# Kernel tuning notes

Hardware: AMD Instinct MI355X
Metric: run time of the kernel (lower is better)

The kernel has to match this reference:

```python
import jax, jax.numpy as jnp
import numpy as np

B, T = 1, 1024
V, E, H, HKV, DH = 32000, 1024, 16, 4, 64
L, R = 2, 2            # n_layer, n_recurrent
ROPE = 32              # head_dim * rotary_pct (0.5)
EPS = 1e-5


def _layer_norm(x, g, b):
    mu = jnp.mean(x, axis=-1, keepdims=True)
    var = jnp.mean((x - mu) ** 2, axis=-1, keepdims=True)
    return (x - mu) * jax.lax.rsqrt(var + EPS) * g + b


def _rotate_half(x):
    x1, x2 = jnp.split(x, 2, axis=-1)
    return jnp.concatenate([-x2, x1], axis=-1)


def _rope_cache(t):
    theta = 1.0 / (10000.0 ** (jnp.arange(0, ROPE, 2, dtype=jnp.float32) / ROPE))
    freqs = jnp.arange(t, dtype=jnp.float32)[:, None] * theta[None, :]  # [t, ROPE/2]
    cos = jnp.concatenate([jnp.cos(freqs), jnp.cos(freqs)], axis=-1)    # [t, ROPE]
    sin = jnp.concatenate([jnp.sin(freqs), jnp.sin(freqs)], axis=-1)
    return cos, sin


def _attn(x, Wq, Wk, Wv, Wo, gate, cos, sin):
    b, t, c = x.shape
    q = (x @ Wq).reshape(b, t, H, DH).transpose(0, 2, 1, 3)     # [b,H,t,D]
    k = (x @ Wk).reshape(b, t, HKV, DH).transpose(0, 2, 1, 3)   # [b,Hkv,t,D]
    v = (x @ Wv).reshape(b, t, HKV, DH).transpose(0, 2, 1, 3)
    c4, s4 = cos[None, None, :t, :], sin[None, None, :t, :]
    q_r, q_p = q[..., :ROPE], q[..., ROPE:]
    k_r, k_p = k[..., :ROPE], k[..., ROPE:]
    q = jnp.concatenate([q_r * c4 + _rotate_half(q_r) * s4, q_p], axis=-1)
    k = jnp.concatenate([k_r * c4 + _rotate_half(k_r) * s4, k_p], axis=-1)
    # GQA: repeat kv heads
    k = jnp.repeat(k, H // HKV, axis=1)
    v = jnp.repeat(v, H // HKV, axis=1)
    att = jnp.einsum('bhtd,bhsd->bhts', q, k) * (DH ** -0.5)
    causal = jnp.tril(jnp.ones((t, t), dtype=bool))
    att = jnp.where(causal[None, None], att, -jnp.inf)
    att = jax.nn.softmax(att, axis=-1)
    # learned per-head sigmoid-threshold sparsifying gate
    thr = jax.nn.sigmoid(gate)[None, :, None, None]
    att = att * (att >= thr).astype(att.dtype)
    y = jnp.einsum('bhts,bhsd->bhtd', att, v).transpose(0, 2, 1, 3).reshape(b, t, c)
    return y @ Wo


def reference(embed, ln1_g, ln1_b, Wq, Wk, Wv, Wo, gate, ln2_g, ln2_b, W1, W2, lnf_g, lnf_b, idx, targets):
    x = embed[idx]                      # [B,T,E]
    cos, sin = _rope_cache(T)
    for _ in range(R):
        for l in range(L):
            x = x + _attn(_layer_norm(x, ln1_g[l], ln1_b[l]), Wq[l], Wk[l], Wv[l], Wo[l], gate[l], cos, sin)
            h = _layer_norm(x, ln2_g[l], ln2_b[l])
            x = x + jax.nn.gelu(h @ W1[l], approximate=False) @ W2[l]
    x = _layer_norm(x, lnf_g, lnf_b)
    logits = x @ embed.T                # tied lm_head
    logp = jax.nn.log_softmax(logits, axis=-1)
    loss = -jnp.mean(jnp.take_along_axis(logp, targets[..., None], axis=-1))
    return logits, loss


def setup_inputs():
    key = jax.random.key(0)
    ks = jax.random.split(key, 9)
    s = 0.02
    return {
        'embed': jax.random.normal(ks[0], (V, E), jnp.float32) * s,
        'ln1_g': jnp.ones((L, E), jnp.float32), 'ln1_b': jnp.zeros((L, E), jnp.float32),
        'Wq': jax.random.normal(ks[1], (L, E, E), jnp.float32) * s,
        'Wk': jax.random.normal(ks[2], (L, E, HKV * DH), jnp.float32) * s,
        'Wv': jax.random.normal(ks[3], (L, E, HKV * DH), jnp.float32) * s,
        'Wo': jax.random.normal(ks[4], (L, E, E), jnp.float32) * s,
        'gate': jnp.zeros((L, H), jnp.float32),
        'ln2_g': jnp.ones((L, E), jnp.float32), 'ln2_b': jnp.zeros((L, E), jnp.float32),
        'W1': jax.random.normal(ks[5], (L, E, 4 * E), jnp.float32) * s,
        'W2': jax.random.normal(ks[6], (L, 4 * E, E), jnp.float32) * s,
        'lnf_g': jnp.ones((E,), jnp.float32), 'lnf_b': jnp.zeros((E,), jnp.float32),
        'idx': jax.random.randint(ks[7], (B, T), 0, V, dtype=jnp.int32),
        'targets': jax.random.randint(ks[8], (B, T), 0, V, dtype=jnp.int32),
    }
```

## Files before the change

### kernel.cpp

```cpp
#include <hip/hip_runtime.h>
#include <math.h>

#define TT 1024
#define VV 32000
#define EE 1024
#define NH 16
#define NKVH 4
#define DHEAD 64
#define QKVN 1536
#define FF 4096
#define LEPS 1e-5f

typedef __attribute__((ext_vector_type(8))) short short8;
typedef __attribute__((ext_vector_type(4))) float floatx4;

__device__ __forceinline__ ushort f2bf(float f) {
    unsigned x = __float_as_uint(f);
    unsigned r = (x + 0x7fffu + ((x >> 16) & 1u)) >> 16;
    return (ushort)r;
}
__device__ __forceinline__ float bf2f(ushort u) {
    return __uint_as_float(((unsigned)u) << 16);
}

__device__ __forceinline__ float block_reduce_sum(float v, float* red) {
    int tid = threadIdx.x;
    red[tid] = v; __syncthreads();
    for (int off = 128; off > 0; off >>= 1) {
        if (tid < off) red[tid] += red[tid + off];
        __syncthreads();
    }
    float r = red[0];
    __syncthreads();
    return r;
}
__device__ __forceinline__ float block_reduce_max(float v, float* red) {
    int tid = threadIdx.x;
    red[tid] = v; __syncthreads();
    for (int off = 128; off > 0; off >>= 1) {
        if (tid < off) red[tid] = fmaxf(red[tid], red[tid + off]);
        __syncthreads();
    }
    float r = red[0];
    __syncthreads();
    return r;
}

__global__ __launch_bounds__(256) void convert_bf16_kernel(const float* __restrict__ src,
                                                           ushort* __restrict__ dst, long n4) {
    long i = (long)blockIdx.x * 256 + threadIdx.x;
    if (i >= n4) return;
    float4 f = ((const float4*)src)[i];
    ushort u[4] = { f2bf(f.x), f2bf(f.y), f2bf(f.z), f2bf(f.w) };
    ((uint2*)dst)[i] = *(uint2*)u;
}

__global__ __launch_bounds__(256) void transpose_bf16_kernel(const float* __restrict__ W,
                                                             ushort* __restrict__ dst,
                                                             int N, int K) {
    __shared__ float tile[32][33];
    int n0 = blockIdx.x * 32, k0 = blockIdx.y * 32;
    int tx = threadIdx.x & 31, ty = threadIdx.x >> 5;
    for (int i = ty; i < 32; i += 8) tile[i][tx] = W[(long)(k0 + i) * N + n0 + tx];
    __syncthreads();
    for (int i = ty; i < 32; i += 8)
        dst[(long)(n0 + i) * K + k0 + tx] = f2bf(tile[tx][i]);
}

__global__ __launch_bounds__(256) void gather_kernel(const float* __restrict__ embed,
                                                     const int* __restrict__ idx,
                                                     float* __restrict__ x) {
    int t = blockIdx.x;
    long r = idx[t];
    const float4* src = (const float4*)(embed + r * EE);
    float4* dst = (float4*)(x + (long)t * EE);
    for (int i = threadIdx.x; i < EE / 4; i += 256) dst[i] = src[i];
}

__global__ __launch_bounds__(256) void ln_kernel(const float* __restrict__ x,
                                                 const float* __restrict__ g,
                                                 const float* __restrict__ b,
                                                 ushort* __restrict__ out) {
    __shared__ float red[256];
    int t = blockIdx.x;
    const float* xr = x + (long)t * EE;
    float s = 0.f;
    for (int i = threadIdx.x; i < EE; i += 256) s += xr[i];
    float mu = block_reduce_sum(s, red) * (1.f / EE);
    float vs = 0.f;
    for (int i = threadIdx.x; i < EE; i += 256) { float d = xr[i] - mu; vs += d * d; }
    float var = block_reduce_sum(vs, red) * (1.f / EE);
    float rstd = rsqrtf(var + LEPS);
    ushort* orow = out + (long)t * EE;
    for (int i = threadIdx.x; i < EE; i += 256)
        orow[i] = f2bf((xr[i] - mu) * rstd * g[i] + b[i]);
}

__global__ __launch_bounds__(256) void reduce_ln_kernel(const float* __restrict__ part,
                                                        float* __restrict__ x,
                                                        const float* __restrict__ g,
                                                        const float* __restrict__ b,
                                                        ushort* __restrict__ out, int SK) {
    __shared__ float red[256];
    int t = blockIdx.x;
    int tid = threadIdx.x;
    float4 v = ((const float4*)(x + (long)t * EE))[tid];
    for (int k = 0; k < SK; ++k) {
        float4 pp = ((const float4*)(part + (long)k * TT * EE + (long)t * EE))[tid];
        v.x += pp.x; v.y += pp.y; v.z += pp.z; v.w += pp.w;
    }
    ((float4*)(x + (long)t * EE))[tid] = v;
    float s = v.x + v.y + v.z + v.w;
    float mu = block_reduce_sum(s, red) * (1.f / EE);
    float d0 = v.x - mu, d1 = v.y - mu, d2 = v.z - mu, d3 = v.w - mu;
    float vs = d0 * d0 + d1 * d1 + d2 * d2 + d3 * d3;
    float var = block_reduce_sum(vs, red) * (1.f / EE);
    float rstd = rsqrtf(var + LEPS);
    float4 gg = ((const float4*)g)[tid];
    float4 bb = ((const float4*)b)[tid];
    ushort4 o;
    o.x = f2bf(d0 * rstd * gg.x + bb.x);
    o.y = f2bf(d1 * rstd * gg.y + bb.y);
    o.z = f2bf(d2 * rstd * gg.z + bb.z);
    o.w = f2bf(d3 * rstd * gg.w + bb.w);
    ((ushort4*)(out + (long)t * EE))[tid] = o;
}

#define M_QKV    0
#define M_FF1    1
#define M_PART   2
#define M_LMHEAD 3

template<int MODE>
__global__ __launch_bounds__(256) void gemm_bf16(const ushort* __restrict__ A,
                                                 const ushort* __restrict__ B,
                                                 void* __restrict__ Cv,
                                                 float* __restrict__ lstats,
                                                 int M, int N, int K) {
    __shared__ char lds[16384];
    const int tid = threadIdx.x;
    const int lane = tid & 63;
    const int w = tid >> 6;

    const int nwg = gridDim.x;
    const int lin = blockIdx.x;
    const int q8 = nwg >> 3, r8 = nwg & 7;
    const int xcd = lin & 7, loc = lin >> 3;
    const int wg = (xcd < r8 ? xcd * (q8 + 1) : r8 * (q8 + 1) + (xcd - r8) * q8) + loc;
    const int MB = M >> 7;
    const int row0 = (wg % MB) * 128;
    const int col0 = (wg / MB) * 128;

    const int nsl = gridDim.y;
    const int kslice = K / nsl;
    const long koff = (long)blockIdx.y * kslice;

    const char* ga[2]; const char* gb[2];
    char* la[2]; char* lb[2];
    #pragma unroll
    for (int r = 0; r < 2; ++r) {
        int c = r * 256 + tid;
        ga[r] = (const char*)A + ((long)(row0 + (c >> 2)) * K + koff) * 2 + (c & 3) * 16;
        gb[r] = (const char*)B + ((long)(col0 + (c >> 2)) * K + koff) * 2 + (c & 3) * 16;
        int wc = r * 256 + w * 64;
        la[r] = lds + wc * 16;
        lb[r] = lds + 8192 + wc * 16;
    }

    floatx4 acc[4][4];
    #pragma unroll
    for (int i = 0; i < 4; ++i)
        #pragma unroll
        for (int j = 0; j < 4; ++j) acc[i][j] = {0.f, 0.f, 0.f, 0.f};

    const int mbase = (w >> 1) * 64;
    const int nbase = (w & 1) * 64;
    const int lr = lane & 15;
    const int ko = (lane >> 4) * 16;

    for (int k0 = 0; k0 < kslice; k0 += 32) {
        #pragma unroll
        for (int r = 0; r < 2; ++r) {
            __builtin_amdgcn_global_load_lds(
                (const __attribute__((address_space(1))) void*)ga[r],
                (__attribute__((address_space(3))) void*)la[r], 16, 0, 0);
            __builtin_amdgcn_global_load_lds(
                (const __attribute__((address_space(1))) void*)gb[r],
                (__attribute__((address_space(3))) void*)lb[r], 16, 0, 0);
            ga[r] += 64; gb[r] += 64;
        }
        __syncthreads();
        short8 af[4], bfr[4];
        #pragma unroll
        for (int i = 0; i < 4; ++i)
            af[i] = *(const short8*)(lds + (mbase + i * 16 + lr) * 64 + ko);
        #pragma unroll
        for (int j = 0; j < 4; ++j)
            bfr[j] = *(const short8*)(lds + 8192 + (nbase + j * 16 + lr) * 64 + ko);
        #pragma unroll
        for (int i = 0; i < 4; ++i)
            #pragma unroll
            for (int j = 0; j < 4; ++j)
                acc[i][j] = __builtin_amdgcn_mfma_f32_16x16x32_bf16(af[i], bfr[j], acc[i][j], 0, 0, 0);
        __syncthreads();
    }

    const int orow = (lane >> 4) * 4;
    const int ocol = lane & 15;

    if (MODE == M_QKV && (col0 + nbase) < (EE + NKVH * DHEAD)) {
        float th = expf(-(float)ocol * 0.5756462732485114f);
        #pragma unroll
        for (int i = 0; i < 4; ++i)
            #pragma unroll
            for (int r = 0; r < 4; ++r) {
                float ang = (float)(row0 + mbase + i * 16 + orow + r) * th;
                float c = cosf(ang), s = sinf(ang);
                float a = acc[i][0][r], bb = acc[i][1][r];
                acc[i][0][r] = a * c - bb * s;
                acc[i][1][r] = bb * c + a * s;
            }
    }

    #pragma unroll
    for (int i = 0; i < 4; ++i) {
        #pragma unroll
        for (int j = 0; j < 4; ++j) {
            #pragma unroll
            for (int r = 0; r < 4; ++r) {
                long off = (long)(row0 + mbase + i * 16 + orow + r) * N
                         + (col0 + nbase + j * 16 + ocol);
                float v = acc[i][j][r];
                if (MODE == M_FF1) v = 0.5f * v * (1.f + erff(v * 0.70710678118654752f));
                if (MODE == M_QKV || MODE == M_FF1) {
                    ((ushort*)Cv)[off] = f2bf(v);
                } else {
                    ((float*)Cv + (long)blockIdx.y * (long)M * N)[off] = v;
                }
            }
        }
    }

    if (MODE == M_LMHEAD) {
        float rm[4][4], rs[4][4];
        #pragma unroll
        for (int i = 0; i < 4; ++i)
            #pragma unroll
            for (int r = 0; r < 4; ++r) {
                float m0 = fmaxf(fmaxf(acc[i][0][r], acc[i][1][r]),
                                 fmaxf(acc[i][2][r], acc[i][3][r]));
                float s0 = expf(acc[i][0][r] - m0) + expf(acc[i][1][r] - m0)
                         + expf(acc[i][2][r] - m0) + expf(acc[i][3][r] - m0);
                #pragma unroll
                for (int off = 1; off < 16; off <<= 1) {
                    float om = __shfl_xor(m0, off);
                    float os = __shfl_xor(s0, off);
                    float nm = fmaxf(m0, om);
                    s0 = s0 * expf(m0 - nm) + os * expf(om - nm);
                    m0 = nm;
                }
                rm[i][r] = m0; rs[i][r] = s0;
            }
        float2* msb = (float2*)lds;
        if (ocol == 0) {
            #pragma unroll
            for (int i = 0; i < 4; ++i)
                #pragma unroll
                for (int r = 0; r < 4; ++r)
                    msb[w * 64 + i * 16 + orow + r] = make_float2(rm[i][r], rs[i][r]);
        }
        __syncthreads();
        if (tid < 128) {
            int half = tid >> 6, rloc = tid & 63;
            float2 a = msb[(half * 2) * 64 + rloc];
            float2 bq = msb[(half * 2 + 1) * 64 + rloc];
            float nm = fmaxf(a.x, bq.x);
            float ns = a.y * expf(a.x - nm) + bq.y * expf(bq.x - nm);
            ((float2*)lstats)[(long)(row0 + half * 64 + rloc) * (N >> 7) + (col0 >> 7)]
                = make_float2(nm, ns);
        }
    }
}

__global__ __launch_bounds__(256) void scores_gemm(const ushort* __restrict__ qkv,
                                                   float* __restrict__ scores) {
    __shared__ char lds[16384];
    const int tid = threadIdx.x;
    const int lane = tid & 63;
    const int w = tid >> 6;
    const int col0 = blockIdx.x * 128, row0 = blockIdx.y * 128, h = blockIdx.z;
    if (col0 > row0) return;

    const ushort* A = qkv + h * DHEAD;
    const ushort* B = qkv + EE + (h >> 2) * DHEAD;

    const char* ga[2]; const char* gb[2];
    char* la[2]; char* lb[2];
    #pragma unroll
    for (int r = 0; r < 2; ++r) {
        int c = r * 256 + tid;
        ga[r] = (const char*)A + (long)(row0 + (c >> 2)) * QKVN * 2 + (c & 3) * 16;
        gb[r] = (const char*)B + (long)(col0 + (c >> 2)) * QKVN * 2 + (c & 3) * 16;
        int wc = r * 256 + w * 64;
        la[r] = lds + wc * 16;
        lb[r] = lds + 8192 + wc * 16;
    }

    floatx4 acc[4][4];
    #pragma unroll
    for (int i = 0; i < 4; ++i)
        #pragma unroll
        for (int j = 0; j < 4; ++j) acc[i][j] = {0.f, 0.f, 0.f, 0.f};

    const int mbase = (w >> 1) * 64;
    const int nbase = (w & 1) * 64;
    const int lr = lane & 15;
    const int ko = (lane >> 4) * 16;

    for (int k0 = 0; k0 < DHEAD; k0 += 32) {
        #pragma unroll
        for (int r = 0; r < 2; ++r) {
            __builtin_amdgcn_global_load_lds(
                (const __attribute__((address_space(1))) void*)ga[r],
                (__attribute__((address_space(3))) void*)la[r], 16, 0, 0);
            __builtin_amdgcn_global_load_lds(
                (const __attribute__((address_space(1))) void*)gb[r],
                (__attribute__((address_space(3))) void*)lb[r], 16, 0, 0);
            ga[r] += 64; gb[r] += 64;
        }
        __syncthreads();
        short8 af[4], bfr[4];
        #pragma unroll
        for (int i = 0; i < 4; ++i)
            af[i] = *(const short8*)(lds + (mbase + i * 16 + lr) * 64 + ko);
        #pragma unroll
        for (int j = 0; j < 4; ++j)
            bfr[j] = *(const short8*)(lds + 8192 + (nbase + j * 16 + lr) * 64 + ko);
        #pragma unroll
        for (int i = 0; i < 4; ++i)
            #pragma unroll
            for (int j = 0; j < 4; ++j)
                acc[i][j] = __builtin_amdgcn_mfma_f32_16x16x32_bf16(af[i], bfr[j], acc[i][j], 0, 0, 0);
        __syncthreads();
    }

    float* C = scores + (long)h * TT * TT;
    const int orow = (lane >> 4) * 4;
    const int ocol = lane & 15;
    #pragma unroll
    for (int i = 0; i < 4; ++i)
        #pragma unroll
        for (int j = 0; j < 4; ++j)
            #pragma unroll
            for (int r = 0; r < 4; ++r)
                C[(long)(row0 + mbase + i * 16 + orow + r) * TT
                  + (col0 + nbase + j * 16 + ocol)] = acc[i][j][r];
}

__global__ __launch_bounds__(256) void softmax_gate_kernel(float* __restrict__ scores,
                                                           const float* __restrict__ gate) {
    int h = blockIdx.x;
    int t = blockIdx.y * 4 + (threadIdx.x >> 6);
    int lane = threadIdx.x & 63;
    float* row = scores + (long)h * TT * TT + (long)t * TT;

    float4 v[4];
    float lmax = -INFINITY;
    #pragma unroll
    for (int q = 0; q < 4; ++q) {
        int u = lane + q * 64;
        v[q] = ((const float4*)row)[u];
        int s0 = u * 4;
        v[q].x = (s0 + 0 <= t) ? v[q].x * 0.125f : -INFINITY;
        v[q].y = (s0 + 1 <= t) ? v[q].y * 0.125f : -INFINITY;
        v[q].z = (s0 + 2 <= t) ? v[q].z * 0.125f : -INFINITY;
        v[q].w = (s0 + 3 <= t) ? v[q].w * 0.125f : -INFINITY;
        lmax = fmaxf(lmax, fmaxf(fmaxf(v[q].x, v[q].y), fmaxf(v[q].z, v[q].w)));
    }
    #pragma unroll
    for (int off = 1; off < 64; off <<= 1)
        lmax = fmaxf(lmax, __shfl_xor(lmax, off));

    float e[16];
    float lsum = 0.f;
    #pragma unroll
    for (int q = 0; q < 4; ++q) {
        e[q * 4 + 0] = expf(v[q].x - lmax);
        e[q * 4 + 1] = expf(v[q].y - lmax);
        e[q * 4 + 2] = expf(v[q].z - lmax);
        e[q * 4 + 3] = expf(v[q].w - lmax);
        lsum += e[q * 4 + 0] + e[q * 4 + 1] + e[q * 4 + 2] + e[q * 4 + 3];
    }
    #pragma unroll
    for (int off = 1; off < 64; off <<= 1)
        lsum += __shfl_xor(lsum, off);

    float inv = 1.f / lsum;
    float thr = 1.f / (1.f + expf(-gate[h]));
    ushort* prow = (ushort*)row;
    #pragma unroll
    for (int q = 0; q < 4; ++q) {
        ushort4 o;
        float p;
        p = e[q * 4 + 0] * inv; o.x = f2bf(p >= thr ? p : 0.f);
        p = e[q * 4 + 1] * inv; o.y = f2bf(p >= thr ? p : 0.f);
        p = e[q * 4 + 2] * inv; o.z = f2bf(p >= thr ? p : 0.f);
        p = e[q * 4 + 3] * inv; o.w = f2bf(p >= thr ? p : 0.f);
        ((ushort4*)prow)[lane + q * 64] = o;
    }
}

__global__ __launch_bounds__(256) void vtrans_kernel(const ushort* __restrict__ qkv,
                                                     ushort* __restrict__ VT) {
    __shared__ ushort tile[32][33];
    int s0 = blockIdx.x * 32, d0 = blockIdx.y * 32;
    int tx = threadIdx.x & 31, ty = threadIdx.x >> 5;
    for (int i = ty; i < 32; i += 8)
        tile[i][tx] = qkv[(long)(s0 + i) * QKVN + (EE + NKVH * DHEAD) + d0 + tx];
    __syncthreads();
    for (int i = ty; i < 32; i += 8)
        VT[(long)(d0 + i) * TT + s0 + tx] = tile[tx][i];
}

__global__ __launch_bounds__(256) void pv_gemm(const float* __restrict__ scores,
                                               const ushort* __restrict__ VT,
                                               ushort* __restrict__ y) {
    __shared__ char lds[12288];
    const int tid = threadIdx.x;
    const int lane = tid & 63;
    const int w = tid >> 6;
    const int row0 = blockIdx.x * 128, h = blockIdx.y;

    const char* Pb = (const char*)(scores + (long)h * TT * TT);
    const char* Bv = (const char*)(VT + (long)(h >> 2) * DHEAD * TT);

    const char* ga[2]; char* la[2];
    #pragma unroll
    for (int r = 0; r < 2; ++r) {
        int c = r * 256 + tid;
        ga[r] = Pb + (long)(row0 + (c >> 2)) * 4096 + (c & 3) * 16;
        la[r] = lds + (r * 256 + w * 64) * 16;
    }
    const char* gb = Bv + (long)(tid >> 2) * 2048 + (tid & 3) * 16;
    char* lb = lds + 8192 + (w * 64) * 16;

    floatx4 acc[2][4];
    #pragma unroll
    for (int i = 0; i < 2; ++i)
        #pragma unroll
        for (int j = 0; j < 4; ++j) acc[i][j] = {0.f, 0.f, 0.f, 0.f};

    const int mbase = w * 32;
    const int lr = lane & 15;
    const int ko = (lane >> 4) * 16;

    const int kmax = row0 + 128;
    for (int k0 = 0; k0 < kmax; k0 += 32) {
        #pragma unroll
        for (int r = 0; r < 2; ++r) {
            __builtin_amdgcn_global_load_lds(
                (const __attribute__((address_space(1))) void*)ga[r],
                (__attribute__((address_space(3))) void*)la[r], 16, 0, 0);
            ga[r] += 64;
        }
        __builtin_amdgcn_global_load_lds(
            (const __attribute__((address_space(1))) void*)gb,
            (__attribute__((address_space(3))) void*)lb, 16, 0, 0);
        gb += 64;
        __syncthreads();
        short8 af[2], bfr[4];
        #pragma unroll
        for (int i = 0; i < 2; ++i)
            af[i] = *(const short8*)(lds + (mbase + i * 16 + lr) * 64 + ko);
        #pragma unroll
        for (int j = 0; j < 4; ++j)
            bfr[j] = *(const short8*)(lds + 8192 + (j * 16 + lr) * 64 + ko);
        #pragma unroll
        for (int i = 0; i < 2; ++i)
            #pragma unroll
            for (int j = 0; j < 4; ++j)
                acc[i][j] = __builtin_amdgcn_mfma_f32_16x16x32_bf16(af[i], bfr[j], acc[i][j], 0, 0, 0);
        __syncthreads();
    }

    const int orow = (lane >> 4) * 4;
    const int ocol = lane & 15;
    #pragma unroll
    for (int i = 0; i < 2; ++i)
        #pragma unroll
        for (int j = 0; j < 4; ++j)
            #pragma unroll
            for (int r = 0; r < 4; ++r)
                y[(long)(row0 + mbase + i * 16 + orow + r) * EE
                  + h * DHEAD + j * 16 + ocol] = f2bf(acc[i][j][r]);
}

__global__ __launch_bounds__(64) void row_loss_kernel(const float* __restrict__ logits,
                                                      const float* __restrict__ lstats,
                                                      const int* __restrict__ targets,
                                                      float* __restrict__ row_loss) {
    int t = blockIdx.x;
    int lane = threadIdx.x;
    const float2* st = (const float2*)lstats + (long)t * (VV / 128);
    float m = -INFINITY, s = 0.f;
    for (int i = lane; i < VV / 128; i += 64) {
        float2 v = st[i];
        float nm = fmaxf(m, v.x);
        s = s * expf(m - nm) + v.y * expf(v.x - nm);
        m = nm;
    }
    #pragma unroll
    for (int off = 1; off < 64; off <<= 1) {
        float om = __shfl_xor(m, off);
        float os = __shfl_xor(s, off);
        float nm = fmaxf(m, om);
        s = s * expf(m - nm) + os * expf(om - nm);
        m = nm;
    }
    if (lane == 0)
        row_loss[t] = logf(s) + m - logits[(long)t * VV + targets[t]];
}

__global__ __launch_bounds__(256) void final_loss_kernel(const float* __restrict__ row_loss,
                                                         float* __restrict__ out) {
    __shared__ float red[256];
    float s = 0.f;
    for (int i = threadIdx.x; i < TT; i += 256) s += row_loss[i];
    float tot = block_reduce_sum(s, red);
    if (threadIdx.x == 0) out[0] = tot * (1.f / TT);
}

extern "C" void kernel_launch(void* const* d_in, const int* in_sizes, int n_in,
                              void* d_out, int out_size, void* d_ws, size_t ws_size,
                              hipStream_t stream) {
    const float* embed = (const float*)d_in[0];
    const float* ln1_g = (const float*)d_in[1];
    const float* ln1_b = (const float*)d_in[2];
    const float* Wq    = (const float*)d_in[3];
    const float* Wk    = (const float*)d_in[4];
    const float* Wv    = (const float*)d_in[5];
    const float* Wo    = (const float*)d_in[6];
    const float* gate  = (const float*)d_in[7];
    const float* ln2_g = (const float*)d_in[8];
    const float* ln2_b = (const float*)d_in[9];
    const float* W1    = (const float*)d_in[10];
    const float* W2    = (const float*)d_in[11];
    const float* lnf_g = (const float*)d_in[12];
    const float* lnf_b = (const float*)d_in[13];
    const int*   idx   = (const int*)d_in[14];
    const int*   tgt   = (const int*)d_in[15];
    float* out = (float*)d_out;

    char* p = (char*)d_ws;
    float*  x      = (float*)p;  p += (long)TT * EE * 4;
    ushort* xn     = (ushort*)p; p += (long)TT * EE * 2;
    ushort* qkvb   = (ushort*)p; p += (long)TT * QKVN * 2;
    ushort* y      = (ushort*)p; p += (long)TT * EE * 2;
    ushort* h1     = (ushort*)p; p += (long)TT * FF * 2;
    float*  rls    = (float*)p;  p += (long)TT * 4;
    ushort* VT     = (ushort*)p; p += (long)NKVH * DHEAD * TT * 2;
    float*  scores = (float*)p;  p += (long)NH * TT * TT * 4;
    ushort* wqkvT  = (ushort*)p; p += (long)2 * QKVN * EE * 2;
    ushort* woT    = (ushort*)p; p += (long)2 * EE * EE * 2;
    ushort* w1T    = (ushort*)p; p += (long)2 * FF * EE * 2;
    ushort* w2T    = (ushort*)p; p += (long)2 * EE * FF * 2;
    ushort* embB   = (ushort*)p; p += (long)VV * EE * 2;

    float* gpart = scores;

    convert_bf16_kernel<<<((long)VV * EE / 4 + 255) / 256, 256, 0, stream>>>(embed, embB, (long)VV * EE / 4);
    for (int l = 0; l < 2; ++l) {
        transpose_bf16_kernel<<<dim3(EE / 32, EE / 32), 256, 0, stream>>>(
            Wq + (long)l * EE * EE, wqkvT + (long)l * QKVN * EE, EE, EE);
        transpose_bf16_kernel<<<dim3(NKVH * DHEAD / 32, EE / 32), 256, 0, stream>>>(
            Wk + (long)l * EE * NKVH * DHEAD, wqkvT + (long)l * QKVN * EE + (long)EE * EE, NKVH * DHEAD, EE);
        transpose_bf16_kernel<<<dim3(NKVH * DHEAD / 32, EE / 32), 256, 0, stream>>>(
            Wv + (long)l * EE * NKVH * DHEAD, wqkvT + (long)l * QKVN * EE + (long)(EE + NKVH * DHEAD) * EE, NKVH * DHEAD, EE);
        transpose_bf16_kernel<<<dim3(EE / 32, EE / 32), 256, 0, stream>>>(
            Wo + (long)l * EE * EE, woT + (long)l * EE * EE, EE, EE);
        transpose_bf16_kernel<<<dim3(FF / 32, EE / 32), 256, 0, stream>>>(
            W1 + (long)l * EE * FF, w1T + (long)l * FF * EE, FF, EE);
        transpose_bf16_kernel<<<dim3(EE / 32, FF / 32), 256, 0, stream>>>(
            W2 + (long)l * FF * EE, w2T + (long)l * EE * FF, EE, FF);
    }

    gather_kernel<<<TT, 256, 0, stream>>>(embed, idx, x);
    ln_kernel<<<TT, 256, 0, stream>>>(x, ln1_g, ln1_b, xn);

    for (int r = 0; r < 2; ++r) {
        for (int l = 0; l < 2; ++l) {
            gemm_bf16<M_QKV><<<dim3((TT / 128) * (QKVN / 128)), 256, 0, stream>>>(
                xn, wqkvT + (long)l * QKVN * EE, qkvb, nullptr, TT, QKVN, EE);
            vtrans_kernel<<<dim3(TT / 32, NKVH * DHEAD / 32), 256, 0, stream>>>(qkvb, VT);
            scores_gemm<<<dim3(TT / 128, TT / 128, NH), 256, 0, stream>>>(qkvb, scores);
            softmax_gate_kernel<<<dim3(NH, TT / 4), 256, 0, stream>>>(scores, gate + l * NH);
            pv_gemm<<<dim3(TT / 128, NH), 256, 0, stream>>>(scores, VT, y);

            gemm_bf16<M_PART><<<dim3((TT / 128) * (EE / 128), 2), 256, 0, stream>>>(
                y, woT + (long)l * EE * EE, gpart, nullptr, TT, EE, EE);
            reduce_ln_kernel<<<TT, 256, 0, stream>>>(
                gpart, x, ln2_g + l * EE, ln2_b + l * EE, xn, 2);

            gemm_bf16<M_FF1><<<dim3((TT / 128) * (FF / 128)), 256, 0, stream>>>(
                xn, w1T + (long)l * FF * EE, h1, nullptr, TT, FF, EE);

            gemm_bf16<M_PART><<<dim3((TT / 128) * (EE / 128), 4), 256, 0, stream>>>(
                h1, w2T + (long)l * EE * FF, gpart, nullptr, TT, EE, FF);
            const float* gn; const float* bn;
            if (r == 1 && l == 1) { gn = lnf_g; bn = lnf_b; }
            else { int lnx = (l == 0) ? 1 : 0; gn = ln1_g + lnx * EE; bn = ln1_b + lnx * EE; }
            reduce_ln_kernel<<<TT, 256, 0, stream>>>(gpart, x, gn, bn, xn, 4);
        }
    }

    gemm_bf16<M_LMHEAD><<<dim3((TT / 128) * (VV / 128)), 256, 0, stream>>>(
        xn, embB, out, gpart, TT, VV, EE);

    row_loss_kernel<<<TT, 64, 0, stream>>>(out, gpart, tgt, rls);
    final_loss_kernel<<<1, 256, 0, stream>>>(rls, out + (long)TT * VV);
}
```

Baseline: 1.186 ms.

## Add dedicated 256x256-tile LM-head GEMM with fused softmax stats

Replaces the generic 128x128 GEMM used for the LM head with a dedicated 512-thread kernel that computes 256x256 tiles. It double-buffers 64-wide K slices into 128KB of LDS via direct global-to-LDS loads with XOR swizzling, and raises wave priority around the MFMA blocks. The per-tile row max and sum-exp are reduced across four column-waves in LDS, giving 125 stats per row instead of 250. The larger tiles raise arithmetic intensity and cut redundant operand reads for the vocabulary GEMM, which is the largest single GEMM here. In exchange the kernel uses heavy LDS and registers, which limits occupancy.

```diff
diff --git a/kernel.cpp b/kernel.cpp
--- a/kernel.cpp
+++ b/kernel.cpp
@@ -129,13 +129,11 @@
 #define M_QKV    0
 #define M_FF1    1
 #define M_PART   2
-#define M_LMHEAD 3
 
 template<int MODE>
 __global__ __launch_bounds__(256) void gemm_bf16(const ushort* __restrict__ A,
                                                  const ushort* __restrict__ B,
                                                  void* __restrict__ Cv,
-                                                 float* __restrict__ lstats,
                                                  int M, int N, int K) {
     __shared__ char lds[16384];
     const int tid = threadIdx.x;
@@ -240,46 +238,156 @@
             }
         }
     }
-
-    if (MODE == M_LMHEAD) {
-        float rm[4][4], rs[4][4];
-        #pragma unroll
-        for (int i = 0; i < 4; ++i)
-            #pragma unroll
-            for (int r = 0; r < 4; ++r) {
-                float m0 = fmaxf(fmaxf(acc[i][0][r], acc[i][1][r]),
-                                 fmaxf(acc[i][2][r], acc[i][3][r]));
-                float s0 = expf(acc[i][0][r] - m0) + expf(acc[i][1][r] - m0)
-                         + expf(acc[i][2][r] - m0) + expf(acc[i][3][r] - m0);
-                #pragma unroll
-                for (int off = 1; off < 16; off <<= 1) {
-                    float om = __shfl_xor(m0, off);
-                    float os = __shfl_xor(s0, off);
-                    float nm = fmaxf(m0, om);
-                    s0 = s0 * expf(m0 - nm) + os * expf(om - nm);
-                    m0 = nm;
-                }
-                rm[i][r] = m0; rs[i][r] = s0;
+}
+
+__global__ __launch_bounds__(512, 2) void lmhead_gemm256(const ushort* __restrict__ A,
+                                                         const ushort* __restrict__ B,
+                                                         float* __restrict__ C,
+                                                         float* __restrict__ lstats) {
+    __shared__ char lds[131072];
+    const int tid = threadIdx.x;
+    const int lane = tid & 63;
+    const int w = tid >> 6;
+    const int wr = w >> 2;
+    const int wc = w & 3;
+
+    const int nwg = gridDim.x;
+    const int lin = blockIdx.x;
+    const int q8 = nwg >> 3, r8 = nwg & 7;
+    const int xcd = lin & 7, loc = lin >> 3;
+    const int wg = (xcd < r8 ? xcd * (q8 + 1) : r8 * (q8 + 1) + (xcd - r8) * q8) + loc;
+    const int row0 = (wg & 3) * 256;
+    const int col0 = (wg >> 2) * 256;
+
+    const int NT = EE / 64;
+
+    const int aB2 = (wr * 128 + (lane & 15)) * 128;
+    const int bB2 = (wc * 64 + (lane & 15)) * 128;
+    const int ks0 = ((0 * 4 + (lane >> 4)) ^ (lane & 7)) * 16;
+    const int ks1 = ((1 * 4 + (lane >> 4)) ^ (lane & 7)) * 16;
+
+    const int sRow = tid >> 3;
+    const int sSlotX = tid & 7;
+
+    floatx4 acc[8][4];
+    #pragma unroll
+    for (int i = 0; i < 8; ++i)
+        #pragma unroll
+        for (int j = 0; j < 4; ++j) acc[i][j] = {0.f, 0.f, 0.f, 0.f};
+
+    #define STAGE256(kt, bufsel)                                                     \
+    do {                                                                             \
+        _Pragma("unroll")                                                            \
+        for (int i = 0; i < 4; ++i) {                                                \
+            int rowD = i * 64 + sRow;                                                \
+            int slotSw = sSlotX ^ (rowD & 7);                                        \
+            const char* gsrc = (const char*)A + (long)(row0 + rowD) * 2048           \
+                             + (kt) * 128 + slotSw * 16;                             \
+            char* ldst = lds + (bufsel) * 32768 + i * 8192 + tid * 16;               \
+            __builtin_amdgcn_global_load_lds(                                        \
+                (const __attribute__((address_space(1))) void*)gsrc,                 \
+                (__attribute__((address_space(3))) void*)ldst, 16, 0, 0);            \
+        }                                                                            \
+        _Pragma("unroll")                                                            \
+        for (int i = 0; i < 4; ++i) {                                                \
+            int rowD = i * 64 + sRow;                                                \
+            int slotSw = sSlotX ^ (rowD & 7);                                        \
+            const char* gsrc = (const char*)B + (long)(col0 + rowD) * 2048           \
+                             + (kt) * 128 + slotSw * 16;                             \
+            char* ldst = lds + 65536 + (bufsel) * 32768 + i * 8192 + tid * 16;       \
+            __builtin_amdgcn_global_load_lds(                                        \
+                (const __attribute__((address_space(1))) void*)gsrc,                 \
+                (__attribute__((address_space(3))) void*)ldst, 16, 0, 0);            \
+        }                                                                            \
+    } while (0)
+
+    STAGE256(0, 0);
+    STAGE256(1, 1);
+    asm volatile("s_waitcnt vmcnt(8)" ::: "memory");
+    __builtin_amdgcn_s_barrier();
+    __builtin_amdgcn_sched_barrier(0);
+
+    for (int kt = 0; kt < NT; ++kt) {
+        const char* Ab = lds + (kt & 1) * 32768;
+        const char* Bb = lds + 65536 + (kt & 1) * 32768;
+
+        short8 bfr[4][2];
+        #pragma unroll
+        for (int fn = 0; fn < 4; ++fn) {
+            bfr[fn][0] = *(const short8*)(Bb + bB2 + fn * 2048 + ks0);
+            bfr[fn][1] = *(const short8*)(Bb + bB2 + fn * 2048 + ks1);
+        }
+        __builtin_amdgcn_s_setprio(1);
+        #pragma unroll
+        for (int fm = 0; fm < 8; ++fm) {
+            short8 a0 = *(const short8*)(Ab + aB2 + fm * 2048 + ks0);
+            short8 a1 = *(const short8*)(Ab + aB2 + fm * 2048 + ks1);
+            #pragma unroll
+            for (int fn = 0; fn < 4; ++fn) {
+                acc[fm][fn] = __builtin_amdgcn_mfma_f32_16x16x32_bf16(a0, bfr[fn][0], acc[fm][fn], 0, 0, 0);
+                acc[fm][fn] = __builtin_amdgcn_mfma_f32_16x16x32_bf16(a1, bfr[fn][1], acc[fm][fn], 0, 0, 0);
             }
-        float2* msb = (float2*)lds;
-        if (ocol == 0) {
-            #pragma unroll
-            for (int i = 0; i < 4; ++i)
-                #pragma unroll
-                for (int r = 0; r < 4; ++r)
-                    msb[w * 64 + i * 16 + orow + r] = make_float2(rm[i][r], rs[i][r]);
-        }
-        __syncthreads();
-        if (tid < 128) {
-            int half = tid >> 6, rloc = tid & 63;
-            float2 a = msb[(half * 2) * 64 + rloc];
-            float2 bq = msb[(half * 2 + 1) * 64 + rloc];
-            float nm = fmaxf(a.x, bq.x);
-            float ns = a.y * expf(a.x - nm) + bq.y * expf(bq.x - nm);
-            ((float2*)lstats)[(long)(row0 + half * 64 + rloc) * (N >> 7) + (col0 >> 7)]
-                = make_float2(nm, ns);
-        }
-    }
+        }
+        __builtin_amdgcn_s_setprio(0);
+
+        if (kt == NT - 1) break;
+
+        asm volatile("s_waitcnt lgkmcnt(0)" ::: "memory");
+        __builtin_amdgcn_s_barrier();
+        __builtin_amdgcn_sched_barrier(0);
+        if (kt + 2 < NT) {
+            STAGE256(kt + 2, kt & 1);
+            asm volatile("s_waitcnt vmcnt(8)" ::: "memory");
+        } else {
+            asm volatile("s_waitcnt vmcnt(0)" ::: "memory");
+        }
+        __builtin_amdgcn_s_barrier();
+        __builtin_amdgcn_sched_barrier(0);
+    }
+    #undef STAGE256
+
+    __syncthreads();
+    float2* msb = (float2*)lds;
+    #pragma unroll
+    for (int fm = 0; fm < 8; ++fm) {
+        #pragma unroll
+        for (int r = 0; r < 4; ++r) {
+            float m0 = fmaxf(fmaxf(acc[fm][0][r], acc[fm][1][r]),
+                             fmaxf(acc[fm][2][r], acc[fm][3][r]));
+            #pragma unroll
+            for (int off = 1; off < 16; off <<= 1)
+                m0 = fmaxf(m0, __shfl_xor(m0, off));
+            float s0 = expf(acc[fm][0][r] - m0) + expf(acc[fm][1][r] - m0)
+                     + expf(acc[fm][2][r] - m0) + expf(acc[fm][3][r] - m0);
+            #pragma unroll
+            for (int off = 1; off < 16; off <<= 1)
+                s0 += __shfl_xor(s0, off);
+            if ((lane & 15) == 0)
+                msb[wc * 256 + wr * 128 + fm * 16 + (lane >> 4) * 4 + r] = make_float2(m0, s0);
+        }
+    }
+    __syncthreads();
+    if (tid < 256) {
+        float2 v = msb[tid];
+        float m = v.x, s = v.y;
+        #pragma unroll
+        for (int q = 1; q < 4; ++q) {
+            float2 u = msb[q * 256 + tid];
+            float nm = fmaxf(m, u.x);
+            s = s * expf(m - nm) + u.y * expf(u.x - nm);
+            m = nm;
+        }
+        ((float2*)lstats)[(long)(row0 + tid) * 125 + (col0 >> 8)] = make_float2(m, s);
+    }
+
+    #pragma unroll
+    for (int fm = 0; fm < 8; ++fm)
+        #pragma unroll
+        for (int fn = 0; fn < 4; ++fn)
+            #pragma unroll
+            for (int r = 0; r < 4; ++r)
+                C[(long)(row0 + wr * 128 + fm * 16 + (lane >> 4) * 4 + r) * VV
+                  + col0 + wc * 64 + fn * 16 + (lane & 15)] = acc[fm][fn][r];
 }
 
 __global__ __launch_bounds__(256) void scores_gemm(const ushort* __restrict__ qkv,
@@ -501,9 +609,9 @@
                                                       float* __restrict__ row_loss) {
     int t = blockIdx.x;
     int lane = threadIdx.x;
-    const float2* st = (const float2*)lstats + (long)t * (VV / 128);
+    const float2* st = (const float2*)lstats + (long)t * 125;
     float m = -INFINITY, s = 0.f;
-    for (int i = lane; i < VV / 128; i += 64) {
+    for (int i = lane; i < 125; i += 64) {
         float2 v = st[i];
         float nm = fmaxf(m, v.x);
         s = s * expf(m - nm) + v.y * expf(v.x - nm);
@@ -590,22 +698,22 @@
     for (int r = 0; r < 2; ++r) {
         for (int l = 0; l < 2; ++l) {
             gemm_bf16<M_QKV><<<dim3((TT / 128) * (QKVN / 128)), 256, 0, stream>>>(
-                xn, wqkvT + (long)l * QKVN * EE, qkvb, nullptr, TT, QKVN, EE);
+                xn, wqkvT + (long)l * QKVN * EE, qkvb, TT, QKVN, EE);
             vtrans_kernel<<<dim3(TT / 32, NKVH * DHEAD / 32), 256, 0, stream>>>(qkvb, VT);
             scores_gemm<<<dim3(TT / 128, TT / 128, NH), 256, 0, stream>>>(qkvb, scores);
             softmax_gate_kernel<<<dim3(NH, TT / 4), 256, 0, stream>>>(scores, gate + l * NH);
             pv_gemm<<<dim3(TT / 128, NH), 256, 0, stream>>>(scores, VT, y);
 
             gemm_bf16<M_PART><<<dim3((TT / 128) * (EE / 128), 2), 256, 0, stream>>>(
-                y, woT + (long)l * EE * EE, gpart, nullptr, TT, EE, EE);
+                y, woT + (long)l * EE * EE, gpart, TT, EE, EE);
             reduce_ln_kernel<<<TT, 256, 0, stream>>>(
                 gpart, x, ln2_g + l * EE, ln2_b + l * EE, xn, 2);
 
             gemm_bf16<M_FF1><<<dim3((TT / 128) * (FF / 128)), 256, 0, stream>>>(
-                xn, w1T + (long)l * FF * EE, h1, nullptr, TT, FF, EE);
+                xn, w1T + (long)l * FF * EE, h1, TT, FF, EE);
 
             gemm_bf16<M_PART><<<dim3((TT / 128) * (EE / 128), 4), 256, 0, stream>>>(
-                h1, w2T + (long)l * EE * FF, gpart, nullptr, TT, EE, FF);
+                h1, w2T + (long)l * EE * FF, gpart, TT, EE, FF);
             const float* gn; const float* bn;
             if (r == 1 && l == 1) { gn = lnf_g; bn = lnf_b; }
             else { int lnx = (l == 0) ? 1 : 0; gn = ln1_g + lnx * EE; bn = ln1_b + lnx * EE; }
@@ -613,8 +721,7 @@
         }
     }
 
-    gemm_bf16<M_LMHEAD><<<dim3((TT / 128) * (VV / 128)), 256, 0, stream>>>(
-        xn, embB, out, gpart, TT, VV, EE);
+    lmhead_gemm256<<<dim3((TT / 256) * (VV / 256)), 512, 0, stream>>>(xn, embB, out, gpart);
 
     row_loss_kernel<<<TT, 64, 0, stream>>>(out, gpart, tgt, rls);
     final_loss_kernel<<<1, 256, 0, stream>>>(rls, out + (long)TT * VV);
```

Result: faster. 1.149 ms (-3.2%).
